# Kernel optimization log

Hardware: AMD Instinct MI355X
Metric: run time of the kernel (lower is better)

## Reference

```python
import jax, jax.numpy as jnp
import numpy as np

IN_CAPS, IN_SIZE = 2401, 8
OUT_CAPS, OUT_SIZE = 8, 16
ROUTING_ITERS = 3


def squash(s, axis):
    mag_sq = jnp.sum(s * s, axis=axis, keepdims=True)
    mag = jnp.sqrt(mag_sq)
    return mag_sq / (1.0 + mag_sq) * (s / mag)


def setup_inputs() -> dict:
    key = jax.random.key(0)
    kx, kw = jax.random.split(key)
    B = 256
    x = jax.random.normal(kx, (B, IN_CAPS, IN_SIZE), dtype=jnp.float32)
    stdv = 1.0 / np.sqrt(IN_CAPS)
    W = jax.random.uniform(kw, (IN_CAPS, OUT_CAPS, OUT_SIZE, IN_SIZE),
                           dtype=jnp.float32, minval=-stdv, maxval=stdv)
    return {"x": x, "W": W}


def reference(x, W):
    # u_hat[b,i,o,c] = W[i,o,c,d] @ x[b,i,d]   -> [B, 2401, 8, 16]
    u_hat = jnp.einsum('iocd,bid->bioc', W, x)
    u_hat_det = jax.lax.stop_gradient(u_hat)

    b_ij = jnp.zeros((IN_CAPS, OUT_CAPS), dtype=x.dtype)
    v_j = None
    for it in range(ROUTING_ITERS):
        c_ij = jax.nn.softmax(b_ij, axis=1)  # softmax over out_capsules
        last = (it == ROUTING_ITERS - 1)
        u = u_hat if last else u_hat_det
        s_j = jnp.einsum('io,bioc->boc', c_ij, u)  # [B, 8, 16]
        v_j = squash(s_j, axis=-1)
        if not last:
            # agreement: mean over batch of <u_hat_i, v_j>
            a = jnp.einsum('bioc,boc->io', u_hat_det, v_j) / x.shape[0]
            b_ij = b_ij + a
    return v_j  # [B, 8, 16]
```

## Files before the change

### kernel.cpp

```cpp
#include <hip/hip_runtime.h>
#include <math.h>

#define IC     2401
#define BSZ    256
#define OC     8
#define CS     16
#define OCC    128
#define XROW   19208
#define KP     19264
#define KTILES 301
#define NI     64

typedef __attribute__((ext_vector_type(8))) short short8;
typedef __attribute__((ext_vector_type(4))) float f32x4;

__device__ __forceinline__ unsigned short f2bf(float f) {
    union { float f; unsigned u; } v; v.f = f;
    const unsigned r = v.u + 0x7FFF + ((v.u >> 16) & 1);
    return (unsigned short)(r >> 16);
}
__device__ __forceinline__ float bf2f(unsigned short h) {
    union { unsigned u; float f; } v; v.u = ((unsigned)h) << 16;
    return v.f;
}

__global__ __launch_bounds__(256)
void prep_kernel(const float* __restrict__ x, const float* __restrict__ W,
                 unsigned short* __restrict__ xT, unsigned short* __restrict__ xB,
                 unsigned short* __restrict__ Wbf, unsigned short* __restrict__ cwt)
{
    const int tid = threadIdx.x;
    if (blockIdx.x < 1204) {
        __shared__ float Ts[64 * 65];
        const int bg = blockIdx.x & 3;
        const int kt = blockIdx.x >> 2;
#pragma unroll
        for (int r = 0; r < 4; ++r) {
            const int flat = r * 256 + tid;
            const int b = flat >> 4, cq = flat & 15;
            const int col = kt * 64 + cq * 4;
            float4 v = make_float4(0.f, 0.f, 0.f, 0.f);
            if (col < XROW) v = *(const float4*)(x + (size_t)(bg * 64 + b) * XROW + col);
            *(float4*)&Ts[b * 65 + cq * 4] = v;
        }
        __syncthreads();
#pragma unroll
        for (int r = 0; r < 2; ++r) {
            const int flat = r * 256 + tid;
            const int rl = flat >> 3, bq = flat & 7;
            union { short8 v; unsigned short h[8]; } o;
#pragma unroll
            for (int j = 0; j < 8; ++j) o.h[j] = f2bf(Ts[(bq * 8 + j) * 65 + rl]);
            *(short8*)(xT + (size_t)(kt * 64 + rl) * 256 + bg * 64 + bq * 8) = o.v;
        }
#pragma unroll
        for (int r = 0; r < 2; ++r) {
            const int flat = r * 256 + tid;
            const int b = flat >> 3, g = flat & 7;
            union { short8 v; unsigned short h[8]; } o;
#pragma unroll
            for (int j = 0; j < 8; ++j) o.h[j] = f2bf(Ts[b * 65 + g * 8 + j]);
            *(short8*)(xB + (size_t)(bg * 64 + b) * KP + (size_t)kt * 64 + g * 8) = o.v;
        }
    } else {
        __shared__ float Ws[8 * 1032];
        const int i0 = (blockIdx.x - 1204) * 8;
#pragma unroll
        for (int r = 0; r < 8; ++r) {
            const int flat = r * 256 + tid;
            const int g = flat >> 8, rem = flat & 255;
            int gi = i0 + g; if (gi > 2400) gi = 2400;
            *(float4*)&Ws[g * 1032 + rem * 4] = *(const float4*)(W + (size_t)gi * 1024 + rem * 4);
        }
        __syncthreads();
#pragma unroll
        for (int r = 0; r < 4; ++r) {
            const int flat = r * 256 + tid;
            const int oc = flat >> 3, g = flat & 7;
            const int gi = i0 + g;
            union { short8 v; unsigned short h[8]; } w, c;
            if (gi <= 2400) {
                const float* wp = &Ws[g * 1032 + oc * 8];
#pragma unroll
                for (int j = 0; j < 8; ++j) { w.h[j] = f2bf(wp[j]); c.h[j] = f2bf(0.125f * wp[j]); }
            } else {
#pragma unroll
                for (int j = 0; j < 8; ++j) { w.h[j] = 0; c.h[j] = 0; }
            }
            *(short8*)(Wbf + (size_t)oc * KP + (size_t)gi * 8) = w.v;
            *(short8*)(cwt + (size_t)oc * KP + (size_t)gi * 8) = c.v;
        }
    }
}

__global__ __launch_bounds__(256)
void s_gemm(const unsigned short* __restrict__ xB, const unsigned short* __restrict__ cwt,
            float* __restrict__ spart)
{
    const int tid = threadIdx.x;
    const int bg  = blockIdx.x, iy = blockIdx.y;
    const int w   = tid >> 6;
    const int ln  = tid & 63;
    const int mr  = ln & 15, qd = ln >> 4;
    const int m0  = bg * 64 + w * 16;

    const unsigned short* ap = xB + (size_t)(m0 + mr) * KP + qd * 8;
    const unsigned short* bp = cwt + (size_t)mr * KP + qd * 8;

    f32x4 acc[8];
#pragma unroll
    for (int n = 0; n < 8; ++n) acc[n] = (f32x4){0.f, 0.f, 0.f, 0.f};

#pragma unroll 1
    for (int kt = iy; kt < KTILES; kt += NI) {
        const int kbase = kt * 64;
#pragma unroll
        for (int kk = 0; kk < 2; ++kk) {
            const int k = kbase + kk * 32;
            const short8 a = *(const short8*)(ap + k);
#pragma unroll
            for (int nt = 0; nt < 8; ++nt) {
                const short8 b = *(const short8*)(bp + (size_t)(nt * 16) * KP + k);
                acc[nt] = __builtin_amdgcn_mfma_f32_16x16x32_bf16(a, b, acc[nt], 0, 0, 0);
            }
        }
    }

    float* op = spart + (size_t)iy * (BSZ * OCC);
#pragma unroll
    for (int nt = 0; nt < 8; ++nt)
#pragma unroll
        for (int r = 0; r < 4; ++r)
            op[(size_t)(m0 + qd * 4 + r) * OCC + nt * 16 + mr] = acc[nt][r];
}

__global__ __launch_bounds__(256)
void squash_kernel(const float* __restrict__ spart, float* __restrict__ vout,
                   unsigned short* __restrict__ vT, int writeT)
{
    __shared__ float red[256];
    const int tid = threadIdx.x;
    const int r0  = blockIdx.x * 8;
    const int idx = tid & 127;
    const int k0  = tid >> 7;

    const float* base = spart + (size_t)r0 * 16 + idx;
    float acc = 0.0f;
#pragma unroll 8
    for (int k = k0; k < NI; k += 2) acc += base[(size_t)k * (BSZ * OCC)];
    red[tid] = acc;
    __syncthreads();

    if (tid < 128) {
        const float s = red[tid] + red[tid + 128];
        float ms = s * s;
        ms += __shfl_xor(ms, 1); ms += __shfl_xor(ms, 2);
        ms += __shfl_xor(ms, 4); ms += __shfl_xor(ms, 8);
        const float scale = sqrtf(ms) / (1.0f + ms);
        const float outv = s * scale;
        const int row = r0 + (tid >> 4);
        const int j   = tid & 15;
        if (writeT) {
            vT[(size_t)((row & 7) * 16 + j) * 256 + (row >> 3)] = f2bf(outv);
        } else {
            vout[(size_t)row * 16 + j] = outv;
        }
    }
}

template<bool FIRST>
__global__ __launch_bounds__(256, 2)
void a_gemm(const unsigned short* __restrict__ xT, const unsigned short* __restrict__ vT,
            const unsigned short* __restrict__ Wbf, float* __restrict__ bij,
            unsigned short* __restrict__ cwt)
{
    __shared__ __align__(16) char smraw[128 * 68 * 4];
    unsigned short* As = (unsigned short*)smraw;
    unsigned short* Bx = (unsigned short*)(smraw + 16384);
    float* Hs = (float*)smraw;

    const int tid = threadIdx.x;
    const int i0  = blockIdx.x * 8;
    const int ln  = tid & 63, wv = tid >> 6;
    const int mr  = ln & 15, qd = ln >> 4;

    f32x4 acc[2][4];
#pragma unroll
    for (int a = 0; a < 2; ++a)
#pragma unroll
        for (int b = 0; b < 4; ++b) acc[a][b] = (f32x4){0.f, 0.f, 0.f, 0.f};

#pragma unroll 1
    for (int bc = 0; bc < 4; ++bc) {
        __syncthreads();
#pragma unroll
        for (int r = 0; r < 4; ++r) {
            const int flat = r * 256 + tid;
            const int oc = flat >> 3, col = flat & 7;
            const short8 v = *(const short8*)(vT + (size_t)oc * 256 + bc * 64 + col * 8);
            *(short8*)&As[oc * 64 + ((col ^ (oc & 7)) * 8)] = v;
        }
#pragma unroll
        for (int r = 0; r < 2; ++r) {
            const int flat = r * 256 + tid;
            const int rw = flat >> 3, col = flat & 7;
            const short8 v = *(const short8*)(xT + (size_t)(i0 * 8 + rw) * 256 + bc * 64 + col * 8);
            *(short8*)&Bx[rw * 64 + ((col ^ (rw & 7)) * 8)] = v;
        }
        __syncthreads();
#pragma unroll
        for (int kk = 0; kk < 2; ++kk) {
            const int csw = ((kk * 4 + qd) ^ (mr & 7)) * 8;
#pragma unroll
            for (int nt = 0; nt < 4; ++nt) {
                const short8 b = *(const short8*)&Bx[(nt * 16 + mr) * 64 + csw];
#pragma unroll
                for (int mt = 0; mt < 2; ++mt) {
                    const short8 a = *(const short8*)&As[((wv * 2 + mt) * 16 + mr) * 64 + csw];
                    acc[mt][nt] = __builtin_amdgcn_mfma_f32_16x16x32_bf16(a, b, acc[mt][nt], 0, 0, 0);
                }
            }
        }
    }

    __syncthreads();
#pragma unroll
    for (int mt = 0; mt < 2; ++mt)
#pragma unroll
        for (int nt = 0; nt < 4; ++nt)
#pragma unroll
            for (int r = 0; r < 4; ++r)
                Hs[((wv * 2 + mt) * 16 + qd * 4 + r) * 68 + nt * 16 + mr] = acc[mt][nt][r];
    __syncthreads();

    const int ch = tid & 3, oo = (tid >> 2) & 7, il = tid >> 5;
    const int ival = i0 + il;
    const int gi = (ival < IC) ? ival : IC - 1;
    const unsigned short* Wt = Wbf + (size_t)(oo * 16 + ch * 4) * KP + (size_t)gi * 8;

    float wreg[4][8];
#pragma unroll
    for (int c = 0; c < 4; ++c) {
        union { short8 v; unsigned short h[8]; } uw;
        uw.v = *(const short8*)(Wt + (size_t)c * KP);
#pragma unroll
        for (int j = 0; j < 8; ++j) wreg[c][j] = bf2f(uw.h[j]);
    }
    float p = 0.0f;
#pragma unroll
    for (int c = 0; c < 4; ++c) {
        const float* hr = &Hs[(oo * 16 + ch * 4 + c) * 68 + il * 8];
        const float4 h0 = *(const float4*)hr;
        const float4 h1 = *(const float4*)(hr + 4);
        p = fmaf(wreg[c][0], h0.x, p); p = fmaf(wreg[c][1], h0.y, p);
        p = fmaf(wreg[c][2], h0.z, p); p = fmaf(wreg[c][3], h0.w, p);
        p = fmaf(wreg[c][4], h1.x, p); p = fmaf(wreg[c][5], h1.y, p);
        p = fmaf(wreg[c][6], h1.z, p); p = fmaf(wreg[c][7], h1.w, p);
    }
    p += __shfl_xor(p, 1); p += __shfl_xor(p, 2);
    const float anew = p * (1.0f / 256.0f);
    float bv = anew;
    if (!FIRST) bv += bij[gi * 8 + oo];
    float mx = bv;
    mx = fmaxf(mx, __shfl_xor(mx, 4));
    mx = fmaxf(mx, __shfl_xor(mx, 8));
    mx = fmaxf(mx, __shfl_xor(mx, 16));
    const float e = expf(bv - mx);
    float ss = e;
    ss += __shfl_xor(ss, 4); ss += __shfl_xor(ss, 8); ss += __shfl_xor(ss, 16);
    float cv = e / ss;
    if (ival >= IC) cv = 0.0f;
    if (ch == 0 && ival < IC) bij[ival * 8 + oo] = bv;
#pragma unroll
    for (int c = 0; c < 4; ++c) {
        union { short8 v; unsigned short h[8]; } o;
#pragma unroll
        for (int j = 0; j < 8; ++j) o.h[j] = f2bf(cv * wreg[c][j]);
        *(short8*)(cwt + (size_t)(oo * 16 + ch * 4 + c) * KP + (size_t)ival * 8) = o.v;
    }
}

extern "C" void kernel_launch(void* const* d_in, const int* in_sizes, int n_in,
                              void* d_out, int out_size, void* d_ws, size_t ws_size,
                              hipStream_t stream)
{
    const float* x = (const float*)d_in[0];
    const float* W = (const float*)d_in[1];
    float* out = (float*)d_out;

    char* p = (char*)d_ws;
    float*          spart = (float*)p;          p += (size_t)NI * BSZ * OCC * 4;
    unsigned short* xT    = (unsigned short*)p; p += (size_t)KP * 256 * 2;
    unsigned short* xB    = (unsigned short*)p; p += (size_t)256 * KP * 2;
    unsigned short* Wbf   = (unsigned short*)p; p += (size_t)128 * KP * 2;
    unsigned short* cwt   = (unsigned short*)p; p += (size_t)128 * KP * 2;
    unsigned short* vT    = (unsigned short*)p; p += (size_t)128 * 256 * 2;
    float*          bij   = (float*)p;

    const dim3 sgrid(4, NI);

    prep_kernel<<<1505, 256, 0, stream>>>(x, W, xT, xB, Wbf, cwt);

    s_gemm<<<sgrid, 256, 0, stream>>>(xB, cwt, spart);
    squash_kernel<<<256, 256, 0, stream>>>(spart, nullptr, vT, 1);
    a_gemm<true><<<KTILES, 256, 0, stream>>>(xT, vT, Wbf, bij, cwt);
    s_gemm<<<sgrid, 256, 0, stream>>>(xB, cwt, spart);
    squash_kernel<<<256, 256, 0, stream>>>(spart, nullptr, vT, 1);
    a_gemm<false><<<KTILES, 256, 0, stream>>>(xT, vT, Wbf, bij, cwt);
    s_gemm<<<sgrid, 256, 0, stream>>>(xB, cwt, spart);
    squash_kernel<<<256, 256, 0, stream>>>(spart, out, vT, 0);
}
```

Before: 153.3 us.

## Fuse all routing stages into one persistent kernel with grid barriers

Replaces the eight separate kernel launches (prep, three s_gemm, three squash, two a_gemm) with a single persistent kernel of 256 blocks that loops over the phases and separates them with atomic-counter grid barriers. The goal is to remove per-launch overhead and inter-kernel gaps. The cost is fewer blocks per phase: prep and a_gemm work now runs as strided loops instead of over 1505 or 301 blocks. Correctness also depends on all 256 blocks being co-resident, and a memset is added to reset the counter.

Result: slower. 581.0 us (+279.0%).

```diff
diff --git a/kernel.cpp b/kernel.cpp
--- a/kernel.cpp
+++ b/kernel.cpp
@@ -10,6 +10,7 @@
 #define KP     19264
 #define KTILES 301
 #define NI     64
+#define NBLK   256
 
 typedef __attribute__((ext_vector_type(8))) short short8;
 typedef __attribute__((ext_vector_type(4))) float f32x4;
@@ -24,85 +25,107 @@
     return v.f;
 }
 
-__global__ __launch_bounds__(256)
-void prep_kernel(const float* __restrict__ x, const float* __restrict__ W,
-                 unsigned short* __restrict__ xT, unsigned short* __restrict__ xB,
-                 unsigned short* __restrict__ Wbf, unsigned short* __restrict__ cwt)
-{
-    const int tid = threadIdx.x;
-    if (blockIdx.x < 1204) {
-        __shared__ float Ts[64 * 65];
-        const int bg = blockIdx.x & 3;
-        const int kt = blockIdx.x >> 2;
-#pragma unroll
-        for (int r = 0; r < 4; ++r) {
-            const int flat = r * 256 + tid;
-            const int b = flat >> 4, cq = flat & 15;
-            const int col = kt * 64 + cq * 4;
-            float4 v = make_float4(0.f, 0.f, 0.f, 0.f);
-            if (col < XROW) v = *(const float4*)(x + (size_t)(bg * 64 + b) * XROW + col);
-            *(float4*)&Ts[b * 65 + cq * 4] = v;
-        }
-        __syncthreads();
-#pragma unroll
-        for (int r = 0; r < 2; ++r) {
-            const int flat = r * 256 + tid;
-            const int rl = flat >> 3, bq = flat & 7;
-            union { short8 v; unsigned short h[8]; } o;
-#pragma unroll
-            for (int j = 0; j < 8; ++j) o.h[j] = f2bf(Ts[(bq * 8 + j) * 65 + rl]);
-            *(short8*)(xT + (size_t)(kt * 64 + rl) * 256 + bg * 64 + bq * 8) = o.v;
-        }
-#pragma unroll
-        for (int r = 0; r < 2; ++r) {
-            const int flat = r * 256 + tid;
-            const int b = flat >> 3, g = flat & 7;
-            union { short8 v; unsigned short h[8]; } o;
-#pragma unroll
-            for (int j = 0; j < 8; ++j) o.h[j] = f2bf(Ts[b * 65 + g * 8 + j]);
-            *(short8*)(xB + (size_t)(bg * 64 + b) * KP + (size_t)kt * 64 + g * 8) = o.v;
-        }
-    } else {
-        __shared__ float Ws[8 * 1032];
-        const int i0 = (blockIdx.x - 1204) * 8;
-#pragma unroll
-        for (int r = 0; r < 8; ++r) {
-            const int flat = r * 256 + tid;
-            const int g = flat >> 8, rem = flat & 255;
-            int gi = i0 + g; if (gi > 2400) gi = 2400;
-            *(float4*)&Ws[g * 1032 + rem * 4] = *(const float4*)(W + (size_t)gi * 1024 + rem * 4);
-        }
-        __syncthreads();
-#pragma unroll
-        for (int r = 0; r < 4; ++r) {
-            const int flat = r * 256 + tid;
-            const int oc = flat >> 3, g = flat & 7;
-            const int gi = i0 + g;
-            union { short8 v; unsigned short h[8]; } w, c;
-            if (gi <= 2400) {
-                const float* wp = &Ws[g * 1032 + oc * 8];
-#pragma unroll
-                for (int j = 0; j < 8; ++j) { w.h[j] = f2bf(wp[j]); c.h[j] = f2bf(0.125f * wp[j]); }
-            } else {
-#pragma unroll
-                for (int j = 0; j < 8; ++j) { w.h[j] = 0; c.h[j] = 0; }
-            }
-            *(short8*)(Wbf + (size_t)oc * KP + (size_t)gi * 8) = w.v;
-            *(short8*)(cwt + (size_t)oc * KP + (size_t)gi * 8) = c.v;
-        }
-    }
-}
-
-__global__ __launch_bounds__(256)
-void s_gemm(const unsigned short* __restrict__ xB, const unsigned short* __restrict__ cwt,
-            float* __restrict__ spart)
-{
-    const int tid = threadIdx.x;
-    const int bg  = blockIdx.x, iy = blockIdx.y;
-    const int w   = tid >> 6;
-    const int ln  = tid & 63;
-    const int mr  = ln & 15, qd = ln >> 4;
-    const int m0  = bg * 64 + w * 16;
+__device__ __forceinline__ void gbar(unsigned* ctr, unsigned target, int tid)
+{
+    __threadfence();
+    __syncthreads();
+    if (tid == 0) {
+        __hip_atomic_fetch_add(ctr, 1u, __ATOMIC_RELAXED, __HIP_MEMORY_SCOPE_AGENT);
+        while (__hip_atomic_load(ctr, __ATOMIC_RELAXED, __HIP_MEMORY_SCOPE_AGENT) < target)
+            __builtin_amdgcn_s_sleep(8);
+    }
+    __syncthreads();
+    __threadfence();
+}
+
+__device__ void phase_prep(char* sm, int blk, int tid,
+                           const float* __restrict__ x, const float* __restrict__ W,
+                           unsigned short* xT, unsigned short* xB,
+                           unsigned short* Wbf, unsigned short* cwt)
+{
+    float* Ts = (float*)sm;
+#pragma unroll 1
+    for (int r = 0; r < 5; ++r) {
+        const int job = blk + NBLK * r;
+        if (job < 1204) {
+            const int bg = job & 3;
+            const int kt = job >> 2;
+            __syncthreads();
+#pragma unroll
+            for (int q = 0; q < 4; ++q) {
+                const int flat = q * 256 + tid;
+                const int b = flat >> 4, cq = flat & 15;
+                const int col = kt * 64 + cq * 4;
+                float4 v = make_float4(0.f, 0.f, 0.f, 0.f);
+                if (col < XROW) v = *(const float4*)(x + (size_t)(bg * 64 + b) * XROW + col);
+                *(float4*)&Ts[b * 65 + cq * 4] = v;
+            }
+            __syncthreads();
+#pragma unroll
+            for (int q = 0; q < 2; ++q) {
+                const int flat = q * 256 + tid;
+                const int rl = flat >> 3, bq = flat & 7;
+                union { short8 v; unsigned short h[8]; } o;
+#pragma unroll
+                for (int j = 0; j < 8; ++j) o.h[j] = f2bf(Ts[(bq * 8 + j) * 65 + rl]);
+                *(short8*)(xT + (size_t)(kt * 64 + rl) * 256 + bg * 64 + bq * 8) = o.v;
+            }
+#pragma unroll
+            for (int q = 0; q < 2; ++q) {
+                const int flat = q * 256 + tid;
+                const int b = flat >> 3, g = flat & 7;
+                union { short8 v; unsigned short h[8]; } o;
+#pragma unroll
+                for (int j = 0; j < 8; ++j) o.h[j] = f2bf(Ts[b * 65 + g * 8 + j]);
+                *(short8*)(xB + (size_t)(bg * 64 + b) * KP + (size_t)kt * 64 + g * 8) = o.v;
+            }
+        }
+    }
+    float* Ws = (float*)sm;
+#pragma unroll 1
+    for (int r = 0; r < 2; ++r) {
+        const int job = blk + NBLK * r;
+        if (job < KTILES) {
+            const int i0 = job * 8;
+            __syncthreads();
+#pragma unroll
+            for (int q = 0; q < 8; ++q) {
+                const int flat = q * 256 + tid;
+                const int g = flat >> 8, rem = flat & 255;
+                int gi = i0 + g; if (gi > 2400) gi = 2400;
+                *(float4*)&Ws[g * 1032 + rem * 4] = *(const float4*)(W + (size_t)gi * 1024 + rem * 4);
+            }
+            __syncthreads();
+#pragma unroll
+            for (int q = 0; q < 4; ++q) {
+                const int flat = q * 256 + tid;
+                const int oc = flat >> 3, g = flat & 7;
+                const int gi = i0 + g;
+                union { short8 v; unsigned short h[8]; } w, c;
+                if (gi <= 2400) {
+                    const float* wp = &Ws[g * 1032 + oc * 8];
+#pragma unroll
+                    for (int j = 0; j < 8; ++j) { w.h[j] = f2bf(wp[j]); c.h[j] = f2bf(0.125f * wp[j]); }
+                } else {
+#pragma unroll
+                    for (int j = 0; j < 8; ++j) { w.h[j] = 0; c.h[j] = 0; }
+                }
+                *(short8*)(Wbf + (size_t)oc * KP + (size_t)gi * 8) = w.v;
+                *(short8*)(cwt + (size_t)oc * KP + (size_t)gi * 8) = c.v;
+            }
+        }
+    }
+}
+
+__device__ void phase_s(int blk, int tid,
+                        const unsigned short* __restrict__ xB,
+                        const unsigned short* __restrict__ cwt, float* spart)
+{
+    const int bg = blk & 3, iy = blk >> 2;
+    const int w  = tid >> 6;
+    const int ln = tid & 63;
+    const int mr = ln & 15, qd = ln >> 4;
+    const int m0 = bg * 64 + w * 16;
 
     const unsigned short* ap = xB + (size_t)(m0 + mr) * KP + qd * 8;
     const unsigned short* bp = cwt + (size_t)mr * KP + qd * 8;
@@ -134,13 +157,11 @@
             op[(size_t)(m0 + qd * 4 + r) * OCC + nt * 16 + mr] = acc[nt][r];
 }
 
-__global__ __launch_bounds__(256)
-void squash_kernel(const float* __restrict__ spart, float* __restrict__ vout,
-                   unsigned short* __restrict__ vT, int writeT)
-{
-    __shared__ float red[256];
-    const int tid = threadIdx.x;
-    const int r0  = blockIdx.x * 8;
+__device__ void phase_v(char* sm, int blk, int tid, const float* __restrict__ spart,
+                        unsigned short* vT, float* out, int writeT)
+{
+    float* red = (float*)sm;
+    const int r0  = blk * 8;
     const int idx = tid & 127;
     const int k0  = tid >> 7;
 
@@ -148,6 +169,7 @@
     float acc = 0.0f;
 #pragma unroll 8
     for (int k = k0; k < NI; k += 2) acc += base[(size_t)k * (BSZ * OCC)];
+    __syncthreads();
     red[tid] = acc;
     __syncthreads();
 
@@ -160,29 +182,24 @@
         const float outv = s * scale;
         const int row = r0 + (tid >> 4);
         const int j   = tid & 15;
-        if (writeT) {
-            vT[(size_t)((row & 7) * 16 + j) * 256 + (row >> 3)] = f2bf(outv);
-        } else {
-            vout[(size_t)row * 16 + j] = outv;
-        }
-    }
-}
-
-template<bool FIRST>
-__global__ __launch_bounds__(256, 2)
-void a_gemm(const unsigned short* __restrict__ xT, const unsigned short* __restrict__ vT,
-            const unsigned short* __restrict__ Wbf, float* __restrict__ bij,
-            unsigned short* __restrict__ cwt)
-{
-    __shared__ __align__(16) char smraw[128 * 68 * 4];
-    unsigned short* As = (unsigned short*)smraw;
-    unsigned short* Bx = (unsigned short*)(smraw + 16384);
-    float* Hs = (float*)smraw;
-
-    const int tid = threadIdx.x;
-    const int i0  = blockIdx.x * 8;
-    const int ln  = tid & 63, wv = tid >> 6;
-    const int mr  = ln & 15, qd = ln >> 4;
+        if (writeT) vT[(size_t)((row & 7) * 16 + j) * 256 + (row >> 3)] = f2bf(outv);
+        else        out[(size_t)row * 16 + j] = outv;
+    }
+}
+
+__device__ void a_job(char* sm, int jb, int tid, int first,
+                      const unsigned short* __restrict__ xT,
+                      const unsigned short* __restrict__ vT,
+                      const unsigned short* __restrict__ Wbf,
+                      float* bij, unsigned short* cwt)
+{
+    unsigned short* As = (unsigned short*)sm;
+    unsigned short* Bx = (unsigned short*)(sm + 16384);
+    float* Hs = (float*)sm;
+
+    const int i0 = jb * 8;
+    const int ln = tid & 63, wv = tid >> 6;
+    const int mr = ln & 15, qd = ln >> 4;
 
     f32x4 acc[2][4];
 #pragma unroll
@@ -260,7 +277,7 @@
     p += __shfl_xor(p, 1); p += __shfl_xor(p, 2);
     const float anew = p * (1.0f / 256.0f);
     float bv = anew;
-    if (!FIRST) bv += bij[gi * 8 + oo];
+    if (!first) bv += bij[gi * 8 + oo];
     float mx = bv;
     mx = fmaxf(mx, __shfl_xor(mx, 4));
     mx = fmaxf(mx, __shfl_xor(mx, 8));
@@ -280,6 +297,34 @@
     }
 }
 
+__global__ __launch_bounds__(256, 2)
+void mega_kernel(const float* __restrict__ x, const float* __restrict__ W,
+                 float* __restrict__ out,
+                 unsigned short* xT, unsigned short* xB, unsigned short* Wbf,
+                 unsigned short* cwt, unsigned short* vT, float* bij,
+                 float* spart, unsigned* ctr)
+{
+    __shared__ __align__(16) char sm[34816];
+    const int blk = blockIdx.x, tid = threadIdx.x;
+    unsigned bar = 0;
+
+    phase_prep(sm, blk, tid, x, W, xT, xB, Wbf, cwt);
+    bar += NBLK; gbar(ctr, bar, tid);
+
+#pragma unroll 1
+    for (int it = 0; it < 3; ++it) {
+        phase_s(blk, tid, xB, cwt, spart);
+        bar += NBLK; gbar(ctr, bar, tid);
+        phase_v(sm, blk, tid, spart, vT, out, it < 2);
+        if (it == 2) break;
+        bar += NBLK; gbar(ctr, bar, tid);
+#pragma unroll 1
+        for (int jb = blk; jb < KTILES; jb += NBLK)
+            a_job(sm, jb, tid, it == 0, xT, vT, Wbf, bij, cwt);
+        bar += NBLK; gbar(ctr, bar, tid);
+    }
+}
+
 extern "C" void kernel_launch(void* const* d_in, const int* in_sizes, int n_in,
                               void* d_out, int out_size, void* d_ws, size_t ws_size,
                               hipStream_t stream)
@@ -289,6 +334,7 @@
     float* out = (float*)d_out;
 
     char* p = (char*)d_ws;
+    unsigned*       ctr   = (unsigned*)p;       p += 256;
     float*          spart = (float*)p;          p += (size_t)NI * BSZ * OCC * 4;
     unsigned short* xT    = (unsigned short*)p; p += (size_t)KP * 256 * 2;
     unsigned short* xB    = (unsigned short*)p; p += (size_t)256 * KP * 2;
@@ -297,16 +343,8 @@
     unsigned short* vT    = (unsigned short*)p; p += (size_t)128 * 256 * 2;
     float*          bij   = (float*)p;
 
-    const dim3 sgrid(4, NI);
-
-    prep_kernel<<<1505, 256, 0, stream>>>(x, W, xT, xB, Wbf, cwt);
-
-    s_gemm<<<sgrid, 256, 0, stream>>>(xB, cwt, spart);
-    squash_kernel<<<256, 256, 0, stream>>>(spart, nullptr, vT, 1);
-    a_gemm<true><<<KTILES, 256, 0, stream>>>(xT, vT, Wbf, bij, cwt);
-    s_gemm<<<sgrid, 256, 0, stream>>>(xB, cwt, spart);
-    squash_kernel<<<256, 256, 0, stream>>>(spart, nullptr, vT, 1);
-    a_gemm<false><<<KTILES, 256, 0, stream>>>(xT, vT, Wbf, bij, cwt);
-    s_gemm<<<sgrid, 256, 0, stream>>>(xB, cwt, spart);
-    squash_kernel<<<256, 256, 0, stream>>>(spart, out, vT, 0);
-}
+    (void)hipMemsetAsync(ctr, 0, 256, stream);
+
+    mega_kernel<<<NBLK, 256, 0, stream>>>(x, W, out, xT, xB, Wbf, cwt, vT, bij,
+                                          spart, ctr);
+}
```
